# Optimization experiments

Hardware: AMD Instinct MI355X
Metric: run time of the kernel (lower is better)

Reference implementation:

```python
import jax, jax.numpy as jnp
import numpy as np

N = 100000
E = 1600000
DIN = 128
HID = 64
DOUT = 40
LAYERS = 8
ALPHA = 0.1
THETA = 0.5


def setup_inputs() -> dict:
    key = jax.random.key(0)
    ks = jax.random.split(key, 8)
    x = jax.random.normal(ks[0], (N, DIN), dtype=jnp.float32)
    edge_index = jax.random.randint(ks[1], (2, E), 0, N, dtype=jnp.int64)
    s1 = 1.0 / np.sqrt(DIN)
    s2 = 1.0 / np.sqrt(HID)
    W1 = jax.random.uniform(ks[2], (DIN, HID), jnp.float32, -s1, s1)
    b1 = jax.random.uniform(ks[3], (HID,), jnp.float32, -s1, s1)
    conv_ws = jax.random.uniform(ks[4], (LAYERS, HID, HID), jnp.float32, -s2, s2)
    W2 = jax.random.uniform(ks[5], (HID, DOUT), jnp.float32, -s2, s2)
    b2 = jax.random.uniform(ks[6], (DOUT,), jnp.float32, -s2, s2)
    return {"x": x, "edge_index": edge_index, "W1": W1, "b1": b1,
            "conv_ws": conv_ws, "W2": W2, "b2": b2}


def reference(x, edge_index, W1, b1, conv_ws, W2, b2):
    n = x.shape[0]
    # gcn_norm with self-loops: Ahat = D^-1/2 (A + I) D^-1/2
    loop = jnp.arange(n, dtype=edge_index.dtype)
    src = jnp.concatenate([edge_index[0], loop])
    dst = jnp.concatenate([edge_index[1], loop])
    deg = jax.ops.segment_sum(jnp.ones_like(src, dtype=x.dtype), dst, num_segments=n)
    dinv = jnp.where(deg > 0, jax.lax.rsqrt(deg), 0.0)
    w_e = dinv[src] * dinv[dst]  # [E+N]

    h0 = h = jax.nn.relu(x @ W1 + b1)  # [N, HID]
    for i in range(LAYERS):
        agg = jax.ops.segment_sum(h[src] * w_e[:, None], dst, num_segments=n)
        out = (1.0 - ALPHA) * agg + ALPHA * h0
        beta = np.log(THETA / (i + 1) + 1.0).astype(np.float32)
        h = jax.nn.relu((1.0 - beta) * out + beta * (out @ conv_ws[i]))
    return h @ W2 + b2
```

## Files before the change

kernel.cpp:

```cpp
#include <hip/hip_runtime.h>
#include <hip/hip_fp16.h>
#include <stdint.h>
#include <math.h>

#define HID 64
#define DIN 128
#define DOUT 40
#define N_LAYERS 8
#define CSR_CAP 768

typedef _Float16 half8 __attribute__((ext_vector_type(8)));
typedef float f32x4 __attribute__((ext_vector_type(4)));

static inline int cdiv(int a, int b) { return (a + b - 1) / b; }

__device__ __forceinline__ int edge_src(const uint32_t* ei, int is64, int E, int e) {
    return is64 ? (int)ei[2 * e] : (int)ei[e];
}
__device__ __forceinline__ int edge_dst(const uint32_t* ei, int is64, int E, int e) {
    return is64 ? (int)ei[2 * (size_t)E + 2 * e] : (int)ei[(size_t)E + e];
}

__global__ void setup(const uint32_t* __restrict__ ei, int* __restrict__ flag,
                      const float* __restrict__ convw, __half* __restrict__ Bp,
                      const float* __restrict__ W1, __half* __restrict__ W1h,
                      const float* __restrict__ W2, __half* __restrict__ W2h,
                      __half* __restrict__ W2l, int* __restrict__ cnt, int n, int nb) {
    int b = blockIdx.x;
    int t = threadIdx.x;
    if (b < nb) {
        int v = b * 256 + t;
        if (v < n) cnt[v] = 0;
        return;
    }
    int r = b - nb;
    if (r < N_LAYERS) {
        float beta = logf(0.5f / (float)(r + 1) + 1.f);
        const float* W = convw + (size_t)r * HID * HID;
        __half* out = Bp + (size_t)r * HID * HID;
        for (int idx = t; idx < HID * HID; idx += 256) {
            int k = idx >> 6, nn = idx & 63;
            float v = beta * W[k * HID + nn] + ((k == nn) ? (1.f - beta) : 0.f);
            out[nn * HID + k] = __float2half(v);
        }
    } else if (r == N_LAYERS) {
        for (int idx = t; idx < DIN * HID; idx += 256) {
            int nn = idx >> 7, k = idx & 127;
            W1h[nn * DIN + k] = __float2half(W1[k * HID + nn]);
        }
    } else if (r == N_LAYERS + 1) {
        if (t < 64) {
            uint32_t wv = ei[2 * t + 1];
            unsigned long long nz = __ballot(wv != 0u);
            if (t == 0) *flag = (nz == 0ull) ? 1 : 0;
        }
    } else {
        for (int idx = t; idx < 48 * 64; idx += 256) {
            int nn = idx >> 6, k = idx & 63;
            float v = (nn < DOUT) ? W2[k * DOUT + nn] : 0.f;
            __half hi = __float2half(v);
            W2h[idx] = hi;
            W2l[idx] = __float2half(v - __half2float(hi));
        }
    }
}

__global__ void count_pos(const uint32_t* __restrict__ ei, const int* __restrict__ flag,
                          int* __restrict__ cnt, int* __restrict__ pw,
                          int e0, int e1, int E) {
    int e = e0 + blockIdx.x * blockDim.x + threadIdx.x;
    if (e >= e1) return;
    int is64 = *flag;
    int d = edge_dst(ei, is64, E, e);
    pw[e] = atomicAdd(&cnt[d], 1);
}

__global__ void scan1(const int* __restrict__ cnt, int* __restrict__ row_start,
                      int* __restrict__ blocksum, int n) {
    __shared__ int sh[256];
    int t = threadIdx.x;
    int v = blockIdx.x * 256 + t;
    int val = (v < n) ? cnt[v] : 0;
    sh[t] = val;
    __syncthreads();
    for (int o = 1; o < 256; o <<= 1) {
        int y = (t >= o) ? sh[t - o] : 0;
        __syncthreads();
        sh[t] += y;
        __syncthreads();
    }
    if (v < n) row_start[v] = sh[t] - val;
    if (t == 255) blocksum[blockIdx.x] = sh[255];
}

__global__ void scan2(int* __restrict__ blocksum, int nb) {
    __shared__ int sh[512];
    int t = threadIdx.x;
    int val = (t < nb) ? blocksum[t] : 0;
    sh[t] = val;
    __syncthreads();
    for (int o = 1; o < 512; o <<= 1) {
        int y = (t >= o) ? sh[t - o] : 0;
        __syncthreads();
        sh[t] += y;
        __syncthreads();
    }
    if (t < nb) blocksum[t] = sh[t] - val;
}

__global__ void scan3(int* __restrict__ row_start, const int* __restrict__ blocksum,
                      const int* __restrict__ cnt, float* __restrict__ dinv, int n) {
    int v = blockIdx.x * 256 + threadIdx.x;
    if (v < n) {
        row_start[v] += blocksum[v >> 8];
        dinv[v] = rsqrtf((float)(cnt[v] + 1));
    }
}

__global__ void scatter_pos(const uint32_t* __restrict__ ei, const int* __restrict__ flag,
                            const int* __restrict__ row_start, const int* __restrict__ pw,
                            int* __restrict__ csr_src, int E) {
    int e = blockIdx.x * blockDim.x + threadIdx.x;
    if (e >= E) return;
    int is64 = *flag;
    int s = edge_src(ei, is64, E, e);
    int d = edge_dst(ei, is64, E, e);
    csr_src[row_start[d] + pw[e]] = s;
}

__global__ void __launch_bounds__(256) mlp_in_mfma(
        const float* __restrict__ x, const __half* __restrict__ W1h,
        const float* __restrict__ b1, const float* __restrict__ dinv,
        __half2* __restrict__ hp2, __half2* __restrict__ h0h2, int n) {
    __shared__ __align__(16) ushort Bs[64 * 136];
    __shared__ __align__(16) ushort As[128 * 136];
    int t = threadIdx.x;
    {
        const __half2* W2v = (const __half2*)W1h;
        for (int i = t; i < 64 * 64; i += 256) {
            int bn = i >> 6, kp = i & 63;
            *(__half2*)&Bs[bn * 136 + 2 * kp] = W2v[bn * 64 + kp];
        }
    }
    int node0 = blockIdx.x * 128;
    {
        const float4* x4 = (const float4*)x;
        for (int i = t; i < 128 * 32; i += 256) {
            int nd = i >> 5, q = i & 31;
            int node = node0 + nd;
            float4 xv = (node < n) ? x4[(size_t)node * 32 + q]
                                   : make_float4(0.f, 0.f, 0.f, 0.f);
            *(__half2*)&As[nd * 136 + q * 4]     = __floats2half2_rn(xv.x, xv.y);
            *(__half2*)&As[nd * 136 + q * 4 + 2] = __floats2half2_rn(xv.z, xv.w);
        }
    }
    __syncthreads();
    int lane = t & 63, wv = t >> 6;
    int nl = lane & 15, quad = lane >> 4;
    int m_base = wv * 32;
    f32x4 C[2][4];
#pragma unroll
    for (int mt = 0; mt < 2; mt++)
#pragma unroll
        for (int nt = 0; nt < 4; nt++) C[mt][nt] = (f32x4)0.f;
#pragma unroll
    for (int kc = 0; kc < 4; kc++) {
        half8 a[2], b[4];
#pragma unroll
        for (int mt = 0; mt < 2; mt++)
            a[mt] = *(const half8*)&As[(m_base + mt * 16 + nl) * 136 + kc * 32 + quad * 8];
#pragma unroll
        for (int nt = 0; nt < 4; nt++)
            b[nt] = *(const half8*)&Bs[(nt * 16 + nl) * 136 + kc * 32 + quad * 8];
#pragma unroll
        for (int mt = 0; mt < 2; mt++)
#pragma unroll
            for (int nt = 0; nt < 4; nt++)
                C[mt][nt] = __builtin_amdgcn_mfma_f32_16x16x32_f16(a[mt], b[nt],
                                                                   C[mt][nt], 0, 0, 0);
    }
    __syncthreads();
#pragma unroll
    for (int nt = 0; nt < 4; nt++) {
        float bias = b1[nt * 16 + nl];
#pragma unroll
        for (int mt = 0; mt < 2; mt++) {
#pragma unroll
            for (int reg = 0; reg < 4; reg++) {
                int nd = m_base + mt * 16 + quad * 4 + reg;
                float v = fmaxf(C[mt][nt][reg] + bias, 0.f);
                As[nd * 72 + nt * 16 + nl] = __half_as_ushort(__float2half(v));
            }
        }
    }
    __syncthreads();
    for (int i = t; i < 128 * 32; i += 256) {
        int nd = i >> 5, kp = i & 31;
        int node = node0 + nd;
        if (node < n) {
            __half2 h = *(const __half2*)&As[nd * 72 + 2 * kp];
            h0h2[(size_t)node * 32 + kp] = h;
            float dv = dinv[node];
            float2 f = __half22float2(h);
            hp2[(size_t)node * 32 + kp] = __floats2half2_rn(f.x * dv, f.y * dv);
        }
    }
}

__global__ void __launch_bounds__(256) gcnii_fused(
        const __half* __restrict__ hp, const __half* __restrict__ h0,
        const int* __restrict__ row_start, const int* __restrict__ csr_src,
        const float* __restrict__ dinv, const __half* __restrict__ Bp,
        const __half* __restrict__ W2h, const __half* __restrict__ W2l,
        const float* __restrict__ b2, int is_last,
        __half* __restrict__ hpn, float* __restrict__ y, int n, int E) {
    __shared__ __align__(16) ushort Bs[64 * 72];
    __shared__ __align__(16) ushort As[32 * 72];
    __shared__ int csr_lds[CSR_CAP];
    __shared__ int rs_lds[33];
    int t = threadIdx.x;
    int node0 = blockIdx.x * 32;
    int grp = t >> 3, sub = t & 7;

    for (int i = t; i < 512; i += 256) {
        int bn = i >> 3, s8 = i & 7;
        *(half8*)&Bs[bn * 72 + s8 * 8] = *(const half8*)(Bp + bn * 64 + s8 * 8);
    }
    int ts = row_start[node0];
    int te = (node0 + 32 < n) ? row_start[node0 + 32] : E;
    int ne = te - ts;
    int staged = ne < CSR_CAP ? ne : CSR_CAP;
    for (int i = t; i < staged; i += 256) csr_lds[i] = csr_src[ts + i];
    if (t < 33) {
        int v = node0 + t;
        rs_lds[t] = ((v < n) ? row_start[v] : E) - ts;
    }
    __syncthreads();

    int v = node0 + grp;
    int j = rs_lds[grp];
    int end = rs_lds[grp + 1];
    float acc[8];
#pragma unroll
    for (int q = 0; q < 8; q++) acc[q] = 0.f;
    if (ne <= CSR_CAP) {
        int e = j;
        for (; e + 4 <= end; e += 4) {
            int s0 = csr_lds[e],     s1 = csr_lds[e + 1];
            int s2 = csr_lds[e + 2], s3 = csr_lds[e + 3];
            if ((unsigned)s0 >= (unsigned)n) s0 = 0;
            if ((unsigned)s1 >= (unsigned)n) s1 = 0;
            if ((unsigned)s2 >= (unsigned)n) s2 = 0;
            if ((unsigned)s3 >= (unsigned)n) s3 = 0;
            half8 h0v = *(const half8*)(hp + (size_t)s0 * 64 + sub * 8);
            half8 h1v = *(const half8*)(hp + (size_t)s1 * 64 + sub * 8);
            half8 h2v = *(const half8*)(hp + (size_t)s2 * 64 + sub * 8);
            half8 h3v = *(const half8*)(hp + (size_t)s3 * 64 + sub * 8);
#pragma unroll
            for (int q = 0; q < 8; q++)
                acc[q] += ((float)h0v[q] + (float)h1v[q]) + ((float)h2v[q] + (float)h3v[q]);
        }
        for (; e < end; ++e) {
            int s = csr_lds[e];
            if ((unsigned)s >= (unsigned)n) s = 0;
            half8 hv = *(const half8*)(hp + (size_t)s * 64 + sub * 8);
#pragma unroll
            for (int q = 0; q < 8; q++) acc[q] += (float)hv[q];
        }
    } else {
        for (int e = j; e < end; ++e) {
            int s = csr_src[ts + e];
            if ((unsigned)s >= (unsigned)n) s = 0;
            half8 hv = *(const half8*)(hp + (size_t)s * 64 + sub * 8);
#pragma unroll
            for (int q = 0; q < 8; q++) acc[q] += (float)hv[q];
        }
    }
    {
        half8 o;
        if (v < n) {
            float sc = 0.9f * dinv[v];
            half8 hsv = *(const half8*)(hp + (size_t)v * 64 + sub * 8);
            half8 h0v = *(const half8*)(h0 + (size_t)v * 64 + sub * 8);
#pragma unroll
            for (int q = 0; q < 8; q++)
                o[q] = (_Float16)(sc * (acc[q] + (float)hsv[q]) + 0.1f * (float)h0v[q]);
        } else {
#pragma unroll
            for (int q = 0; q < 8; q++) o[q] = (_Float16)0.f;
        }
        *(half8*)&As[grp * 72 + sub * 8] = o;
    }
    __syncthreads();
    int lane = t & 63, w = t >> 6;
    int nl = lane & 15, quad = lane >> 4;
    int strip = w & 1, nth = w >> 1;
    f32x4 C[2];
    C[0] = (f32x4)0.f; C[1] = (f32x4)0.f;
#pragma unroll
    for (int kc = 0; kc < 2; kc++) {
        half8 a = *(const half8*)&As[(strip * 16 + nl) * 72 + kc * 32 + quad * 8];
#pragma unroll
        for (int t2 = 0; t2 < 2; t2++) {
            int nt = nth * 2 + t2;
            half8 b = *(const half8*)&Bs[(nt * 16 + nl) * 72 + kc * 32 + quad * 8];
            C[t2] = __builtin_amdgcn_mfma_f32_16x16x32_f16(a, b, C[t2], 0, 0, 0);
        }
    }
    __syncthreads();
#pragma unroll
    for (int reg = 0; reg < 4; reg++) {
        int nd = strip * 16 + quad * 4 + reg;
        int node = node0 + nd;
        float dv = (!is_last && node < n) ? dinv[node] : 1.f;
#pragma unroll
        for (int t2 = 0; t2 < 2; t2++) {
            int nt = nth * 2 + t2;
            float vv = fmaxf(C[t2][reg], 0.f) * dv;
            As[nd * 72 + nt * 16 + nl] = __half_as_ushort(__float2half(vv));
        }
    }
    __syncthreads();
    if (!is_last) {
        int nd = t >> 3, s8 = t & 7;
        int node = node0 + nd;
        if (node < n)
            *(half8*)(hpn + (size_t)node * 64 + s8 * 8) = *(const half8*)&As[nd * 72 + s8 * 8];
    } else {
        for (int ct = nth; ct < 3; ct += 2) {
            f32x4 C2 = (f32x4)0.f;
#pragma unroll
            for (int kc = 0; kc < 2; kc++) {
                half8 a  = *(const half8*)&As[(strip * 16 + nl) * 72 + kc * 32 + quad * 8];
                half8 bh = *(const half8*)(W2h + (ct * 16 + nl) * 64 + kc * 32 + quad * 8);
                half8 bl = *(const half8*)(W2l + (ct * 16 + nl) * 64 + kc * 32 + quad * 8);
                C2 = __builtin_amdgcn_mfma_f32_16x16x32_f16(a, bh, C2, 0, 0, 0);
                C2 = __builtin_amdgcn_mfma_f32_16x16x32_f16(a, bl, C2, 0, 0, 0);
            }
            int col = ct * 16 + nl;
            float bias = (col < DOUT) ? b2[col] : 0.f;
#pragma unroll
            for (int reg = 0; reg < 4; reg++) {
                int nd = strip * 16 + quad * 4 + reg;
                int node = node0 + nd;
                if (node < n && col < DOUT)
                    y[(size_t)node * DOUT + col] = C2[reg] + bias;
            }
        }
    }
}

extern "C" void kernel_launch(void* const* d_in, const int* in_sizes, int n_in,
                              void* d_out, int out_size, void* d_ws, size_t ws_size,
                              hipStream_t stream) {
    const float*    x     = (const float*)d_in[0];
    const uint32_t* ei    = (const uint32_t*)d_in[1];
    const float*    W1    = (const float*)d_in[2];
    const float*    b1    = (const float*)d_in[3];
    const float*    convw = (const float*)d_in[4];
    const float*    W2    = (const float*)d_in[5];
    const float*    b2    = (const float*)d_in[6];
    float*          y     = (float*)d_out;

    int N = in_sizes[0] / DIN;
    int E = in_sizes[1] / 2;

    char* ws = (char*)d_ws;
    size_t off = 0;
    auto alloc = [&](size_t bytes) -> char* {
        char* p = ws + off;
        off = (off + bytes + 255) & ~(size_t)255;
        return p;
    };
    int*     flag      = (int*)alloc(4);
    int*     cnt       = (int*)alloc((size_t)N * 4);
    int*     row_start = (int*)alloc((size_t)N * 4);
    float*   dinv      = (float*)alloc((size_t)N * 4);
    int*     blocksum  = (int*)alloc(512 * 4);
    int*     pw        = (int*)alloc((size_t)E * 4);
    int*     csr_src   = (int*)alloc((size_t)E * 4);
    __half*  Bp        = (__half*)alloc((size_t)N_LAYERS * HID * HID * 2);
    __half*  W1h       = (__half*)alloc((size_t)DIN * HID * 2);
    __half*  W2h       = (__half*)alloc((size_t)48 * HID * 2);
    __half*  W2l       = (__half*)alloc((size_t)48 * HID * 2);
    __half*  h0h       = (__half*)alloc((size_t)N * HID * 2);
    __half*  hpA       = (__half*)alloc((size_t)N * HID * 2);
    __half*  hpB       = (__half*)alloc((size_t)N * HID * 2);

    int nb = cdiv(N, 256);
    setup<<<nb + N_LAYERS + 3, 256, 0, stream>>>(ei, flag, convw, Bp, W1, W1h,
                                                 W2, W2h, W2l, cnt, N, nb);
    int Eh = E / 2;
    count_pos<<<cdiv(Eh, 256), 256, 0, stream>>>(ei, flag, cnt, pw, 0, Eh, E);
    count_pos<<<cdiv(E - Eh, 256), 256, 0, stream>>>(ei, flag, cnt, pw, Eh, E, E);
    scan1<<<nb, 256, 0, stream>>>(cnt, row_start, blocksum, N);
    scan2<<<1, 512, 0, stream>>>(blocksum, nb);
    scan3<<<cdiv(N, 256), 256, 0, stream>>>(row_start, blocksum, cnt, dinv, N);
    scatter_pos<<<cdiv(E, 256), 256, 0, stream>>>(ei, flag, row_start, pw, csr_src, E);

    mlp_in_mfma<<<cdiv(N, 128), 256, 0, stream>>>(x, W1h, b1, dinv,
                                                  (__half2*)hpA, (__half2*)h0h, N);

    __half* cur = hpA;
    __half* nxt = hpB;
    for (int i = 0; i < N_LAYERS; i++) {
        int is_last = (i == N_LAYERS - 1) ? 1 : 0;
        gcnii_fused<<<cdiv(N, 32), 256, 0, stream>>>(
            cur, h0h, row_start, csr_src, dinv,
            Bp + (size_t)i * HID * HID, W2h, W2l, b2, is_last, nxt, y, N, E);
        __half* tmp = cur; cur = nxt; nxt = tmp;
    }
}
```

Before: 501.6 us.

## Process 64 nodes per 512-thread block, unroll gathers by 8, prefetch self features

The fused GCNII layer kernel now handles 64 destination nodes per block with 512 threads, so each block loads the 64x64 weight tile once for twice as many nodes. The CSR staging capacity doubles to match. The neighbor gather loop is unrolled to 8 independent half8 loads to expose more memory-level parallelism, and the node's own features, h0 and dinv are loaded before the barrier to overlap them with staging. The costs are more LDS and register use per block, which may lower occupancy.

```diff
diff --git a/kernel.cpp b/kernel.cpp
--- a/kernel.cpp
+++ b/kernel.cpp
@@ -7,7 +7,7 @@
 #define DIN 128
 #define DOUT 40
 #define N_LAYERS 8
-#define CSR_CAP 768
+#define CSR_CAP 1536
 
 typedef _Float16 half8 __attribute__((ext_vector_type(8)));
 typedef float f32x4 __attribute__((ext_vector_type(4)));
@@ -207,7 +207,7 @@
     }
 }
 
-__global__ void __launch_bounds__(256) gcnii_fused(
+__global__ void __launch_bounds__(512) gcnii_fused(
         const __half* __restrict__ hp, const __half* __restrict__ h0,
         const int* __restrict__ row_start, const int* __restrict__ csr_src,
         const float* __restrict__ dinv, const __half* __restrict__ Bp,
@@ -215,29 +215,34 @@
         const float* __restrict__ b2, int is_last,
         __half* __restrict__ hpn, float* __restrict__ y, int n, int E) {
     __shared__ __align__(16) ushort Bs[64 * 72];
-    __shared__ __align__(16) ushort As[32 * 72];
+    __shared__ __align__(16) ushort As[64 * 72];
     __shared__ int csr_lds[CSR_CAP];
-    __shared__ int rs_lds[33];
+    __shared__ int rs_lds[65];
     int t = threadIdx.x;
-    int node0 = blockIdx.x * 32;
+    int node0 = blockIdx.x * 64;
     int grp = t >> 3, sub = t & 7;
 
-    for (int i = t; i < 512; i += 256) {
-        int bn = i >> 3, s8 = i & 7;
-        *(half8*)&Bs[bn * 72 + s8 * 8] = *(const half8*)(Bp + bn * 64 + s8 * 8);
-    }
     int ts = row_start[node0];
-    int te = (node0 + 32 < n) ? row_start[node0 + 32] : E;
+    int te = (node0 + 64 < n) ? row_start[node0 + 64] : E;
     int ne = te - ts;
     int staged = ne < CSR_CAP ? ne : CSR_CAP;
-    for (int i = t; i < staged; i += 256) csr_lds[i] = csr_src[ts + i];
-    if (t < 33) {
+    for (int i = t; i < staged; i += 512) csr_lds[i] = csr_src[ts + i];
+    if (t < 65) {
         int v = node0 + t;
         rs_lds[t] = ((v < n) ? row_start[v] : E) - ts;
     }
-    __syncthreads();
-
+    {
+        int bn = t >> 3, s8 = t & 7;
+        *(half8*)&Bs[bn * 72 + s8 * 8] = *(const half8*)(Bp + bn * 64 + s8 * 8);
+    }
     int v = node0 + grp;
+    bool valid = (v < n);
+    int vc = valid ? v : 0;
+    half8 hsv = *(const half8*)(hp + (size_t)vc * 64 + sub * 8);
+    half8 h0v = *(const half8*)(h0 + (size_t)vc * 64 + sub * 8);
+    float dvv = dinv[vc];
+    __syncthreads();
+
     int j = rs_lds[grp];
     int end = rs_lds[grp + 1];
     float acc[8];
@@ -245,20 +250,39 @@
     for (int q = 0; q < 8; q++) acc[q] = 0.f;
     if (ne <= CSR_CAP) {
         int e = j;
-        for (; e + 4 <= end; e += 4) {
+        for (; e + 8 <= end; e += 8) {
+            int s[8];
+#pragma unroll
+            for (int u = 0; u < 8; u++) {
+                s[u] = csr_lds[e + u];
+                if ((unsigned)s[u] >= (unsigned)n) s[u] = 0;
+            }
+            half8 hv[8];
+#pragma unroll
+            for (int u = 0; u < 8; u++)
+                hv[u] = *(const half8*)(hp + (size_t)s[u] * 64 + sub * 8);
+#pragma unroll
+            for (int q = 0; q < 8; q++)
+                acc[q] += (((float)hv[0][q] + (float)hv[1][q]) +
+                           ((float)hv[2][q] + (float)hv[3][q])) +
+                          (((float)hv[4][q] + (float)hv[5][q]) +
+                           ((float)hv[6][q] + (float)hv[7][q]));
+        }
+        if (e + 4 <= end) {
             int s0 = csr_lds[e],     s1 = csr_lds[e + 1];
             int s2 = csr_lds[e + 2], s3 = csr_lds[e + 3];
             if ((unsigned)s0 >= (unsigned)n) s0 = 0;
             if ((unsigned)s1 >= (unsigned)n) s1 = 0;
             if ((unsigned)s2 >= (unsigned)n) s2 = 0;
             if ((unsigned)s3 >= (unsigned)n) s3 = 0;
-            half8 h0v = *(const half8*)(hp + (size_t)s0 * 64 + sub * 8);
-            half8 h1v = *(const half8*)(hp + (size_t)s1 * 64 + sub * 8);
-            half8 h2v = *(const half8*)(hp + (size_t)s2 * 64 + sub * 8);
-            half8 h3v = *(const half8*)(hp + (size_t)s3 * 64 + sub * 8);
+            half8 a0 = *(const half8*)(hp + (size_t)s0 * 64 + sub * 8);
+            half8 a1 = *(const half8*)(hp + (size_t)s1 * 64 + sub * 8);
+            half8 a2 = *(const half8*)(hp + (size_t)s2 * 64 + sub * 8);
+            half8 a3 = *(const half8*)(hp + (size_t)s3 * 64 + sub * 8);
 #pragma unroll
             for (int q = 0; q < 8; q++)
-                acc[q] += ((float)h0v[q] + (float)h1v[q]) + ((float)h2v[q] + (float)h3v[q]);
+                acc[q] += ((float)a0[q] + (float)a1[q]) + ((float)a2[q] + (float)a3[q]);
+            e += 4;
         }
         for (; e < end; ++e) {
             int s = csr_lds[e];
@@ -278,10 +302,8 @@
     }
     {
         half8 o;
-        if (v < n) {
-            float sc = 0.9f * dinv[v];
-            half8 hsv = *(const half8*)(hp + (size_t)v * 64 + sub * 8);
-            half8 h0v = *(const half8*)(h0 + (size_t)v * 64 + sub * 8);
+        if (valid) {
+            float sc = 0.9f * dvv;
 #pragma unroll
             for (int q = 0; q < 8; q++)
                 o[q] = (_Float16)(sc * (acc[q] + (float)hsv[q]) + 0.1f * (float)h0v[q]);
@@ -294,7 +316,7 @@
     __syncthreads();
     int lane = t & 63, w = t >> 6;
     int nl = lane & 15, quad = lane >> 4;
-    int strip = w & 1, nth = w >> 1;
+    int strip = w & 3, half = w >> 2;
     f32x4 C[2];
     C[0] = (f32x4)0.f; C[1] = (f32x4)0.f;
 #pragma unroll
@@ -302,7 +324,7 @@
         half8 a = *(const half8*)&As[(strip * 16 + nl) * 72 + kc * 32 + quad * 8];
 #pragma unroll
         for (int t2 = 0; t2 < 2; t2++) {
-            int nt = nth * 2 + t2;
+            int nt = half * 2 + t2;
             half8 b = *(const half8*)&Bs[(nt * 16 + nl) * 72 + kc * 32 + quad * 8];
             C[t2] = __builtin_amdgcn_mfma_f32_16x16x32_f16(a, b, C[t2], 0, 0, 0);
         }
@@ -315,7 +337,7 @@
         float dv = (!is_last && node < n) ? dinv[node] : 1.f;
 #pragma unroll
         for (int t2 = 0; t2 < 2; t2++) {
-            int nt = nth * 2 + t2;
+            int nt = half * 2 + t2;
             float vv = fmaxf(C[t2][reg], 0.f) * dv;
             As[nd * 72 + nt * 16 + nl] = __half_as_ushort(__float2half(vv));
         }
@@ -327,7 +349,7 @@
         if (node < n)
             *(half8*)(hpn + (size_t)node * 64 + s8 * 8) = *(const half8*)&As[nd * 72 + s8 * 8];
     } else {
-        for (int ct = nth; ct < 3; ct += 2) {
+        for (int ct = half; ct < 3; ct += 2) {
             f32x4 C2 = (f32x4)0.f;
 #pragma unroll
             for (int kc = 0; kc < 2; kc++) {
@@ -405,7 +427,7 @@
     __half* nxt = hpB;
     for (int i = 0; i < N_LAYERS; i++) {
         int is_last = (i == N_LAYERS - 1) ? 1 : 0;
-        gcnii_fused<<<cdiv(N, 32), 256, 0, stream>>>(
+        gcnii_fused<<<cdiv(N, 64), 512, 0, stream>>>(
             cur, h0h, row_start, csr_src, dinv,
             Bp + (size_t)i * HID * HID, W2h, W2l, b2, is_last, nxt, y, N, E);
         __half* tmp = cur; cur = nxt; nxt = tmp;
```

Result: slower. 540.7 us (+7.8%).

## Fuse input MLP with edge counting and dinv scaling with CSR scatter

Applied to the files above, without the earlier changes.

The input MLP no longer waits for the degree scan. It runs in the same launch as the edge-count atomics, using separate block ranges, and writes only h0. The dinv scaling of h0 into hp moves into the scatter kernel as extra grid-stride blocks. This cuts the number of launches and lets independent work overlap. In exchange, h0 is read back once more, and the MLP now uses 64-node tiles that read B directly from global memory instead of staging it in LDS.

```diff
diff --git a/kernel.cpp b/kernel.cpp
--- a/kernel.cpp
+++ b/kernel.cpp
@@ -65,14 +65,69 @@
     }
 }
 
-__global__ void count_pos(const uint32_t* __restrict__ ei, const int* __restrict__ flag,
-                          int* __restrict__ cnt, int* __restrict__ pw,
-                          int e0, int e1, int E) {
-    int e = e0 + blockIdx.x * blockDim.x + threadIdx.x;
-    if (e >= e1) return;
-    int is64 = *flag;
-    int d = edge_dst(ei, is64, E, e);
-    pw[e] = atomicAdd(&cnt[d], 1);
+__global__ void __launch_bounds__(256) count_mlp(
+        const uint32_t* __restrict__ ei, const int* __restrict__ flag,
+        int* __restrict__ cnt, int* __restrict__ pw, int E,
+        const float* __restrict__ x, const __half* __restrict__ W1h,
+        const float* __restrict__ b1, __half2* __restrict__ h0h2, int n, int GC) {
+    __shared__ __align__(16) ushort As[64 * 136];
+    int b = blockIdx.x;
+    int t = threadIdx.x;
+    if (b < GC) {
+        int e = b * 256 + t;
+        if (e < E) {
+            int is64 = *flag;
+            int d = edge_dst(ei, is64, E, e);
+            pw[e] = atomicAdd(&cnt[d], 1);
+        }
+        return;
+    }
+    int node0 = (b - GC) * 64;
+    {
+        const float4* x4 = (const float4*)x;
+        for (int i = t; i < 64 * 32; i += 256) {
+            int nd = i >> 5, q = i & 31;
+            int node = node0 + nd;
+            float4 xv = (node < n) ? x4[(size_t)node * 32 + q]
+                                   : make_float4(0.f, 0.f, 0.f, 0.f);
+            *(__half2*)&As[nd * 136 + q * 4]     = __floats2half2_rn(xv.x, xv.y);
+            *(__half2*)&As[nd * 136 + q * 4 + 2] = __floats2half2_rn(xv.z, xv.w);
+        }
+    }
+    __syncthreads();
+    int lane = t & 63, wv = t >> 6;
+    int nl = lane & 15, quad = lane >> 4;
+    int m_base = wv * 16;
+    f32x4 C[4];
+#pragma unroll
+    for (int nt = 0; nt < 4; nt++) C[nt] = (f32x4)0.f;
+#pragma unroll
+    for (int kc = 0; kc < 4; kc++) {
+        half8 a = *(const half8*)&As[(m_base + nl) * 136 + kc * 32 + quad * 8];
+#pragma unroll
+        for (int nt = 0; nt < 4; nt++) {
+            half8 bb = *(const half8*)(W1h + (nt * 16 + nl) * DIN + kc * 32 + quad * 8);
+            C[nt] = __builtin_amdgcn_mfma_f32_16x16x32_f16(a, bb, C[nt], 0, 0, 0);
+        }
+    }
+    __syncthreads();
+#pragma unroll
+    for (int nt = 0; nt < 4; nt++) {
+        float bias = b1[nt * 16 + nl];
+#pragma unroll
+        for (int reg = 0; reg < 4; reg++) {
+            int nd = m_base + quad * 4 + reg;
+            float v = fmaxf(C[nt][reg] + bias, 0.f);
+            As[nd * 72 + nt * 16 + nl] = __half_as_ushort(__float2half(v));
+        }
+    }
+    __syncthreads();
+    for (int i = t; i < 64 * 32; i += 256) {
+        int nd = i >> 5, kp = i & 31;
+        int node = node0 + nd;
+        if (node < n)
+            h0h2[(size_t)node * 32 + kp] = *(const __half2*)&As[nd * 72 + 2 * kp];
+    }
 }
 
 __global__ void scan1(const int* __restrict__ cnt, int* __restrict__ row_start,
@@ -117,93 +172,30 @@
     }
 }
 
-__global__ void scatter_pos(const uint32_t* __restrict__ ei, const int* __restrict__ flag,
-                            const int* __restrict__ row_start, const int* __restrict__ pw,
-                            int* __restrict__ csr_src, int E) {
-    int e = blockIdx.x * blockDim.x + threadIdx.x;
-    if (e >= E) return;
-    int is64 = *flag;
-    int s = edge_src(ei, is64, E, e);
-    int d = edge_dst(ei, is64, E, e);
-    csr_src[row_start[d] + pw[e]] = s;
-}
-
-__global__ void __launch_bounds__(256) mlp_in_mfma(
-        const float* __restrict__ x, const __half* __restrict__ W1h,
-        const float* __restrict__ b1, const float* __restrict__ dinv,
-        __half2* __restrict__ hp2, __half2* __restrict__ h0h2, int n) {
-    __shared__ __align__(16) ushort Bs[64 * 136];
-    __shared__ __align__(16) ushort As[128 * 136];
-    int t = threadIdx.x;
-    {
-        const __half2* W2v = (const __half2*)W1h;
-        for (int i = t; i < 64 * 64; i += 256) {
-            int bn = i >> 6, kp = i & 63;
-            *(__half2*)&Bs[bn * 136 + 2 * kp] = W2v[bn * 64 + kp];
-        }
-    }
-    int node0 = blockIdx.x * 128;
-    {
-        const float4* x4 = (const float4*)x;
-        for (int i = t; i < 128 * 32; i += 256) {
-            int nd = i >> 5, q = i & 31;
-            int node = node0 + nd;
-            float4 xv = (node < n) ? x4[(size_t)node * 32 + q]
-                                   : make_float4(0.f, 0.f, 0.f, 0.f);
-            *(__half2*)&As[nd * 136 + q * 4]     = __floats2half2_rn(xv.x, xv.y);
-            *(__half2*)&As[nd * 136 + q * 4 + 2] = __floats2half2_rn(xv.z, xv.w);
-        }
-    }
-    __syncthreads();
-    int lane = t & 63, wv = t >> 6;
-    int nl = lane & 15, quad = lane >> 4;
-    int m_base = wv * 32;
-    f32x4 C[2][4];
-#pragma unroll
-    for (int mt = 0; mt < 2; mt++)
-#pragma unroll
-        for (int nt = 0; nt < 4; nt++) C[mt][nt] = (f32x4)0.f;
-#pragma unroll
-    for (int kc = 0; kc < 4; kc++) {
-        half8 a[2], b[4];
-#pragma unroll
-        for (int mt = 0; mt < 2; mt++)
-            a[mt] = *(const half8*)&As[(m_base + mt * 16 + nl) * 136 + kc * 32 + quad * 8];
-#pragma unroll
-        for (int nt = 0; nt < 4; nt++)
-            b[nt] = *(const half8*)&Bs[(nt * 16 + nl) * 136 + kc * 32 + quad * 8];
-#pragma unroll
-        for (int mt = 0; mt < 2; mt++)
-#pragma unroll
-            for (int nt = 0; nt < 4; nt++)
-                C[mt][nt] = __builtin_amdgcn_mfma_f32_16x16x32_f16(a[mt], b[nt],
-                                                                   C[mt][nt], 0, 0, 0);
-    }
-    __syncthreads();
-#pragma unroll
-    for (int nt = 0; nt < 4; nt++) {
-        float bias = b1[nt * 16 + nl];
-#pragma unroll
-        for (int mt = 0; mt < 2; mt++) {
-#pragma unroll
-            for (int reg = 0; reg < 4; reg++) {
-                int nd = m_base + mt * 16 + quad * 4 + reg;
-                float v = fmaxf(C[mt][nt][reg] + bias, 0.f);
-                As[nd * 72 + nt * 16 + nl] = __half_as_ushort(__float2half(v));
-            }
-        }
-    }
-    __syncthreads();
-    for (int i = t; i < 128 * 32; i += 256) {
-        int nd = i >> 5, kp = i & 31;
-        int node = node0 + nd;
-        if (node < n) {
-            __half2 h = *(const __half2*)&As[nd * 72 + 2 * kp];
-            h0h2[(size_t)node * 32 + kp] = h;
-            float dv = dinv[node];
-            float2 f = __half22float2(h);
-            hp2[(size_t)node * 32 + kp] = __floats2half2_rn(f.x * dv, f.y * dv);
-        }
+__global__ void __launch_bounds__(256) scatter_hp(
+        const uint32_t* __restrict__ ei, const int* __restrict__ flag,
+        const int* __restrict__ row_start, const int* __restrict__ pw,
+        int* __restrict__ csr_src, int E,
+        const __half2* __restrict__ h0h2, const float* __restrict__ dinv,
+        __half2* __restrict__ hp2, int n, int GS, int GH) {
+    int b = blockIdx.x;
+    int t = threadIdx.x;
+    if (b < GS) {
+        int e = b * 256 + t;
+        if (e < E) {
+            int is64 = *flag;
+            int s = edge_src(ei, is64, E, e);
+            int d = edge_dst(ei, is64, E, e);
+            csr_src[row_start[d] + pw[e]] = s;
+        }
+        return;
+    }
+    int total = n * 32;
+    for (int idx = (b - GS) * 256 + t; idx < total; idx += GH * 256) {
+        int node = idx >> 5;
+        float dv = dinv[node];
+        float2 f = __half22float2(h0h2[idx]);
+        hp2[idx] = __floats2half2_rn(f.x * dv, f.y * dv);
     }
 }
 
@@ -390,16 +382,18 @@
     int nb = cdiv(N, 256);
     setup<<<nb + N_LAYERS + 3, 256, 0, stream>>>(ei, flag, convw, Bp, W1, W1h,
                                                  W2, W2h, W2l, cnt, N, nb);
-    int Eh = E / 2;
-    count_pos<<<cdiv(Eh, 256), 256, 0, stream>>>(ei, flag, cnt, pw, 0, Eh, E);
-    count_pos<<<cdiv(E - Eh, 256), 256, 0, stream>>>(ei, flag, cnt, pw, Eh, E, E);
+    int GC = cdiv(E, 256);
+    int GM = cdiv(N, 64);
+    count_mlp<<<GC + GM, 256, 0, stream>>>(ei, flag, cnt, pw, E,
+                                           x, W1h, b1, (__half2*)h0h, N, GC);
     scan1<<<nb, 256, 0, stream>>>(cnt, row_start, blocksum, N);
     scan2<<<1, 512, 0, stream>>>(blocksum, nb);
     scan3<<<cdiv(N, 256), 256, 0, stream>>>(row_start, blocksum, cnt, dinv, N);
-    scatter_pos<<<cdiv(E, 256), 256, 0, stream>>>(ei, flag, row_start, pw, csr_src, E);
-
-    mlp_in_mfma<<<cdiv(N, 128), 256, 0, stream>>>(x, W1h, b1, dinv,
-                                                  (__half2*)hpA, (__half2*)h0h, N);
+    int GS = cdiv(E, 256);
+    int GH = 512;
+    scatter_hp<<<GS + GH, 256, 0, stream>>>(ei, flag, row_start, pw, csr_src, E,
+                                            (const __half2*)h0h, dinv,
+                                            (__half2*)hpA, N, GS, GH);
 
     __half* cur = hpA;
     __half* nxt = hpB;
```

Result: no change. 500.0 us (-0.3%).
